# Performance work log

Hardware: AMD Instinct MI355X
Metric: run time of the kernel (lower is better)

Reference implementation:

```python
import jax, jax.numpy as jnp
import numpy as np
import math

B, CIN, H, W = 32, 128, 64, 64
COUT, KH, KW = 256, 3, 3


def setup_inputs() -> dict:
    key = jax.random.key(0)
    k1, k2, k3 = jax.random.split(key, 3)
    sqrtk = math.sqrt(1.0 / (CIN * KH * KW))
    x = jax.random.normal(k1, (B, CIN, H, W), dtype=jnp.float32)
    weight = jax.random.uniform(k2, (COUT, CIN, KH, KW), dtype=jnp.float32, minval=-sqrtk, maxval=sqrtk)
    bias = jax.random.uniform(k3, (COUT,), dtype=jnp.float32, minval=-sqrtk, maxval=sqrtk)
    return {"input": x, "weight": weight, "bias": bias}


def reference(input, weight, bias):
    # VALID (no padding), stride-1 cross-correlation conv, NCHW/OIHW layout,
    # matching the original nested-loop direct convolution + per-channel bias.
    out = jax.lax.conv_general_dilated(
        input, weight,
        window_strides=(1, 1), padding='VALID',
        dimension_numbers=('NCHW', 'OIHW', 'NCHW'))
    return out + bias[None, :, None, None]
```

## Files before the change

kernel.cpp:

```cpp
#include <hip/hip_runtime.h>

#define NB   32
#define NCI  128
#define NH   64
#define NW   64
#define NCO  256
#define NOH  62
#define NOW  62

typedef __attribute__((ext_vector_type(8))) short bf16x8;
typedef __attribute__((ext_vector_type(8))) unsigned short u16x8;
typedef __attribute__((ext_vector_type(4))) float f32x4;

typedef __attribute__((address_space(1))) const unsigned int glb_u32_t;
typedef __attribute__((address_space(3))) unsigned int lds_u32_t;

__device__ __forceinline__ unsigned short f2bf(float f) {
  unsigned int u = __float_as_uint(f);
  u = u + 0x7FFFu + ((u >> 16) & 1u);
  return (unsigned short)(u >> 16);
}

__device__ __forceinline__ void gload_lds16(const unsigned short* g, unsigned short* l) {
  __builtin_amdgcn_global_load_lds((glb_u32_t*)g, (lds_u32_t*)l, 16, 0, 0);
}

__global__ __launch_bounds__(256) void cvt_w_kernel(const float* __restrict__ wsrc,
                                                    unsigned short* __restrict__ wt) {
  int t = blockIdx.x * 256 + threadIdx.x;
  int oc = t & 15, co = (t >> 4) & 255, k = t >> 12;
  const float* src = wsrc + ((size_t)co * NCI + oc * 8) * 9 + k;
  u16x8 v;
  #pragma unroll
  for (int j = 0; j < 8; ++j) v[j] = f2bf(src[j * 9]);
  *(u16x8*)(wt + ((size_t)k * NCO + co) * NCI + oc * 8) = v;
}

__global__ __launch_bounds__(256, 2) void conv_mfma_kernel(
    const float* __restrict__ x, const unsigned short* __restrict__ wt,
    const float* __restrict__ bias, float* __restrict__ out) {
  __shared__ unsigned short smem[40960];

  const int tid  = threadIdx.x;
  const int lane = tid & 63;
  const int wid  = tid >> 6;
  const int wn   = wid;
  const int l15  = lane & 15;
  const int lo   = lane >> 4;

  const int bid0  = blockIdx.x;
  const int bid   = (bid0 & 7) * 128 + (bid0 >> 3);
  const int coutg = bid & 1;
  const int ohg   = (bid >> 1) & 15;
  const int b     = bid >> 5;
  const int cbase = coutg * 128;
  const int oh0   = ohg * 4;

  f32x4 acc[8][4];
  #pragma unroll
  for (int mi = 0; mi < 8; ++mi)
    #pragma unroll
    for (int ni = 0; ni < 4; ++ni)
      acc[mi][ni] = (f32x4){0.f, 0.f, 0.f, 0.f};

  const char* sm = (const char*)smem;
  const int af_lane = l15 * 64 + ((lo ^ ((l15 >> 1) & 3)) << 4);

  const float* xb = x + ((size_t)b * NCI) * (NH * NW);

  const unsigned short* wsrc2[2];
  #pragma unroll
  for (int i = 0; i < 2; ++i) {
    int e = (wid * 2 + i) * 64 + lane;
    int o = e & 3, co = e >> 2;
    wsrc2[i] = wt + (size_t)(cbase + co) * NCI + ((o ^ ((co >> 1) & 3)) * 8);
  }

  auto stage_w = [&](int t) {
    unsigned short* dst = smem + 24576 + (t & 3) * 4096;
    const size_t so = (size_t)(t % 9) * NCO * NCI + (t / 9) * 32;
    #pragma unroll
    for (int i = 0; i < 2; ++i)
      gload_lds16(wsrc2[i] + so, dst + ((wid * 2 + i) * 64 + lane) * 8);
  };

  auto xload8 = [&](int c1, int uu, float (&xf)[8]) {
    const int g = uu * 4 + wid;
    const int r = g % 6, oct = g / 6;
    int row = oh0 + r; if (row > 63) row = 63;
    const float* src = xb + (size_t)(c1 * 32 + oct * 8) * (NH * NW)
                     + row * NW + lane;
    #pragma unroll
    for (int j = 0; j < 8; ++j) xf[j] = src[(size_t)j * (NH * NW)];
  };
  auto xwrite8 = [&](int c1, int uu, float (&xf)[8]) {
    const int g = uu * 4 + wid;
    const int r = g % 6, oct = g / 6;
    u16x8 v;
    #pragma unroll
    for (int j = 0; j < 8; ++j) v[j] = f2bf(xf[j]);
    *(u16x8*)(smem + (c1 & 1) * 12288 +
              ((r * 64 + lane) * 4 + (oct ^ ((lane >> 1) & 3))) * 8) = v;
  };

  bf16x8 afX[4], afY[4], bfC[4];

  {
    float xa[8], xbv[8], xc[8], xd[8], xe[8], xg[8];
    xload8(0, 0, xa); xload8(0, 1, xbv); xload8(0, 2, xc);
    xload8(0, 3, xd); xload8(0, 4, xe);  xload8(0, 5, xg);
    stage_w(0); stage_w(1); stage_w(2);
    asm volatile("s_waitcnt vmcnt(6)" ::: "memory");
    xwrite8(0, 0, xa); xwrite8(0, 1, xbv); xwrite8(0, 2, xc);
    xwrite8(0, 3, xd); xwrite8(0, 4, xe);  xwrite8(0, 5, xg);
    asm volatile("s_waitcnt vmcnt(0) lgkmcnt(0)" ::: "memory");
    __builtin_amdgcn_s_barrier();
    __builtin_amdgcn_sched_barrier(0);
    const char* wsp0 = sm + 49152;
    #pragma unroll
    for (int i = 0; i < 4; ++i)
      afX[i] = *(const bf16x8*)(wsp0 + i * 1024 + af_lane);
    const char* xsp0 = sm + wn * 4096;
    #pragma unroll
    for (int i = 0; i < 4; ++i)
      bfC[i] = *(const bf16x8*)(xsp0 + i * 1024 + af_lane);
  }

  for (int t = 0; t < 36; ++t) {
    const int t9 = t % 9, c = t / 9;
    const bool xst = (t9 >= 2 && t9 <= 7) && (c < 3);
    const bool pf  = (t < 35);
    float xf[8];

    if (xst) xload8(c + 1, t9 - 2, xf);
    __builtin_amdgcn_sched_barrier(0);
    if (t + 3 < 36) stage_w(t + 3);
    __builtin_amdgcn_sched_barrier(0);

    const char* wsp  = sm + 49152 + (t & 3) * 8192;
    const char* wspn = sm + 49152 + ((t + 1) & 3) * 8192;

    asm volatile("s_waitcnt lgkmcnt(0)" ::: "memory");
    __builtin_amdgcn_sched_barrier(0);
    __builtin_amdgcn_s_setprio(1);
    #pragma unroll
    for (int ni = 0; ni < 4; ++ni)
      acc[0][ni] = __builtin_amdgcn_mfma_f32_16x16x32_bf16(afX[0], bfC[ni], acc[0][ni], 0, 0, 0);
    afY[0] = *(const bf16x8*)(wsp + 4 * 1024 + af_lane);
    afY[1] = *(const bf16x8*)(wsp + 5 * 1024 + af_lane);
    #pragma unroll
    for (int ni = 0; ni < 4; ++ni)
      acc[1][ni] = __builtin_amdgcn_mfma_f32_16x16x32_bf16(afX[1], bfC[ni], acc[1][ni], 0, 0, 0);
    afY[2] = *(const bf16x8*)(wsp + 6 * 1024 + af_lane);
    afY[3] = *(const bf16x8*)(wsp + 7 * 1024 + af_lane);
    #pragma unroll
    for (int ni = 0; ni < 4; ++ni)
      acc[2][ni] = __builtin_amdgcn_mfma_f32_16x16x32_bf16(afX[2], bfC[ni], acc[2][ni], 0, 0, 0);
    #pragma unroll
    for (int ni = 0; ni < 4; ++ni)
      acc[3][ni] = __builtin_amdgcn_mfma_f32_16x16x32_bf16(afX[3], bfC[ni], acc[3][ni], 0, 0, 0);
    __builtin_amdgcn_s_setprio(0);

    asm volatile("s_waitcnt lgkmcnt(0)" ::: "memory");
    __builtin_amdgcn_sched_barrier(0);
    __builtin_amdgcn_s_setprio(1);
    #pragma unroll
    for (int ni = 0; ni < 4; ++ni)
      acc[4][ni] = __builtin_amdgcn_mfma_f32_16x16x32_bf16(afY[0], bfC[ni], acc[4][ni], 0, 0, 0);
    if (pf) {
      afX[0] = *(const bf16x8*)(wspn + 0 * 1024 + af_lane);
      afX[1] = *(const bf16x8*)(wspn + 1 * 1024 + af_lane);
    }
    #pragma unroll
    for (int ni = 0; ni < 4; ++ni)
      acc[5][ni] = __builtin_amdgcn_mfma_f32_16x16x32_bf16(afY[1], bfC[ni], acc[5][ni], 0, 0, 0);
    if (pf) {
      afX[2] = *(const bf16x8*)(wspn + 2 * 1024 + af_lane);
      afX[3] = *(const bf16x8*)(wspn + 3 * 1024 + af_lane);
    }
    #pragma unroll
    for (int ni = 0; ni < 4; ++ni)
      acc[6][ni] = __builtin_amdgcn_mfma_f32_16x16x32_bf16(afY[2], bfC[ni], acc[6][ni], 0, 0, 0);
    #pragma unroll
    for (int ni = 0; ni < 4; ++ni)
      acc[7][ni] = __builtin_amdgcn_mfma_f32_16x16x32_bf16(afY[3], bfC[ni], acc[7][ni], 0, 0, 0);
    __builtin_amdgcn_s_setprio(0);

    if (t >= 33) {
      asm volatile("s_waitcnt vmcnt(0)" ::: "memory");
    } else {
      asm volatile("s_waitcnt vmcnt(2)" ::: "memory");
    }
    if (xst) xwrite8(c + 1, t9 - 2, xf);
    if (pf) {
      const int tn = t + 1, tn9 = tn % 9, cn = tn / 9;
      const int khn = tn9 / 3, kwn = tn9 - khn * 3;
      const char* xspn = sm + (cn & 1) * 24576 + (wn + khn) * 4096;
      const int w9n = l15 + kwn;
      const int bfln = w9n * 64 + ((lo ^ ((w9n >> 1) & 3)) << 4);
      #pragma unroll
      for (int i = 0; i < 4; ++i)
        bfC[i] = *(const bf16x8*)(xspn + i * 1024 + bfln);
    }
    if (xst) asm volatile("s_waitcnt lgkmcnt(4)" ::: "memory");
    __builtin_amdgcn_s_barrier();
    __builtin_amdgcn_sched_barrier(0);
  }

  const int oh = oh0 + wn;
  if (oh < NOH) {
    #pragma unroll
    for (int mi = 0; mi < 8; ++mi) {
      int co0 = cbase + mi * 16 + lo * 4;
      const f32x4 bv = *(const f32x4*)(bias + co0);
      #pragma unroll
      for (int ni = 0; ni < 4; ++ni) {
        int ow = ni * 16 + l15;
        if (ow < NOW) {
          size_t o0 = (((size_t)b * NCO + co0) * NOH + oh) * NOW + ow;
          const size_t cs = (size_t)NOH * NOW;
          out[o0]          = acc[mi][ni][0] + bv[0];
          out[o0 + cs]     = acc[mi][ni][1] + bv[1];
          out[o0 + 2 * cs] = acc[mi][ni][2] + bv[2];
          out[o0 + 3 * cs] = acc[mi][ni][3] + bv[3];
        }
      }
    }
  }
}

__global__ __launch_bounds__(256) void conv_naive_kernel(
    const float* __restrict__ x, const float* __restrict__ w,
    const float* __restrict__ bias, float* __restrict__ out) {
  long t = (long)blockIdx.x * 256 + threadIdx.x;
  const long total = (long)NB * NCO * NOH * NOW;
  if (t >= total) return;
  int ow = (int)(t % NOW);
  int oh = (int)((t / NOW) % NOH);
  int co = (int)((t / ((long)NOW * NOH)) % NCO);
  int b  = (int)(t / ((long)NOW * NOH * NCO));
  float acc = bias[co];
  for (int ci = 0; ci < NCI; ++ci) {
    const float* xp = x + (((size_t)b * NCI + ci) * NH + oh) * NW + ow;
    const float* wp = w + ((size_t)co * NCI + ci) * 9;
    #pragma unroll
    for (int kh = 0; kh < 3; ++kh)
      #pragma unroll
      for (int kw = 0; kw < 3; ++kw)
        acc += xp[kh * NW + kw] * wp[kh * 3 + kw];
  }
  out[t] = acc;
}

extern "C" void kernel_launch(void* const* d_in, const int* in_sizes, int n_in,
                              void* d_out, int out_size, void* d_ws, size_t ws_size,
                              hipStream_t stream) {
  const float* x    = (const float*)d_in[0];
  const float* w    = (const float*)d_in[1];
  const float* bias = (const float*)d_in[2];
  float* out        = (float*)d_out;

  const size_t WT_BYTES = (size_t)9 * NCO * NCI * 2;

  if (ws_size >= WT_BYTES) {
    unsigned short* wt = (unsigned short*)d_ws;
    cvt_w_kernel<<<(9 * NCO * 16) / 256, 256, 0, stream>>>(w, wt);
    conv_mfma_kernel<<<2 * 16 * NB, 256, 0, stream>>>(x, wt, bias, out);
  } else {
    const long total = (long)NB * NCO * NOH * NOW;
    conv_naive_kernel<<<(int)((total + 255) / 256), 256, 0, stream>>>(x, w, bias, out);
  }
}
```

Baseline: 88.83 us.

## Switch conv main loop to 32x32x16 bf16 MFMA with double-buffered B fragments

Replaces the 16x16x32 MFMA tiling (8x4 accumulators) with 32x32x16 MFMA (4x2 accumulators of 16 floats). The LDS fragment addressing and the output epilogue are remapped to match. The tap loop becomes a lambda unrolled four times and ping-pongs two B-fragment register sets, so next-tap input fragments load during the current MFMAs rather than after them. The aim is fewer MFMA issues and fewer LDS reads per tap, with B-fragment load latency hidden. In exchange the larger unrolled body may raise register pressure, and the new swizzle mapping must stay correct.

```diff
diff --git a/kernel.cpp b/kernel.cpp
--- a/kernel.cpp
+++ b/kernel.cpp
@@ -8,9 +8,10 @@
 #define NOH  62
 #define NOW  62
 
-typedef __attribute__((ext_vector_type(8))) short bf16x8;
-typedef __attribute__((ext_vector_type(8))) unsigned short u16x8;
-typedef __attribute__((ext_vector_type(4))) float f32x4;
+typedef __attribute__((ext_vector_type(8)))  short bf16x8;
+typedef __attribute__((ext_vector_type(8)))  unsigned short u16x8;
+typedef __attribute__((ext_vector_type(4)))  float f32x4;
+typedef __attribute__((ext_vector_type(16))) float f32x16;
 
 typedef __attribute__((address_space(1))) const unsigned int glb_u32_t;
 typedef __attribute__((address_space(3))) unsigned int lds_u32_t;
@@ -45,8 +46,8 @@
   const int lane = tid & 63;
   const int wid  = tid >> 6;
   const int wn   = wid;
-  const int l15  = lane & 15;
-  const int lo   = lane >> 4;
+  const int l31  = lane & 31;
+  const int lo5  = lane >> 5;
 
   const int bid0  = blockIdx.x;
   const int bid   = (bid0 & 7) * 128 + (bid0 >> 3);
@@ -56,15 +57,16 @@
   const int cbase = coutg * 128;
   const int oh0   = ohg * 4;
 
-  f32x4 acc[8][4];
+  f32x16 acc[4][2];
   #pragma unroll
-  for (int mi = 0; mi < 8; ++mi)
-    #pragma unroll
-    for (int ni = 0; ni < 4; ++ni)
-      acc[mi][ni] = (f32x4){0.f, 0.f, 0.f, 0.f};
+  for (int mi = 0; mi < 4; ++mi)
+    #pragma unroll
+    for (int ni = 0; ni < 2; ++ni)
+      acc[mi][ni] = (f32x16)(0.f);
 
   const char* sm = (const char*)smem;
-  const int af_lane = l15 * 64 + ((lo ^ ((l15 >> 1) & 3)) << 4);
+  const int afb0 = l31 * 64 + ((lo5 ^ ((l31 >> 1) & 3)) << 4);
+  const int afb1 = afb0 ^ 32;
 
   const float* xb = x + ((size_t)b * NCI) * (NH * NW);
 
@@ -103,7 +105,73 @@
               ((r * 64 + lane) * 4 + (oct ^ ((lane >> 1) & 3))) * 8) = v;
   };
 
-  bf16x8 afX[4], afY[4], bfC[4];
+  bf16x8 afX[4], afY[4], bfC[4], bfD[4];
+
+  auto tap_body = [&](int t, bf16x8 (&bfc)[4], bf16x8 (&bfn)[4], bool pf) {
+    const int t9 = t % 9, c = t / 9;
+    const bool xst = (t9 >= 2 && t9 <= 7) && (c < 3);
+    float xf[8];
+
+    if (xst) xload8(c + 1, t9 - 2, xf);
+    __builtin_amdgcn_sched_barrier(0);
+    if (t + 3 < 36) stage_w(t + 3);
+    __builtin_amdgcn_sched_barrier(0);
+
+    const char* wsp  = sm + 49152 + (t & 3) * 8192;
+    const char* wspn = sm + 49152 + ((t + 1) & 3) * 8192;
+    const int tn = t + 1, tn9 = tn % 9, cn = tn / 9;
+    const int khn = tn9 / 3, kwn = tn9 - khn * 3;
+    const char* xspn = sm + (cn & 1) * 24576 + (wn + khn) * 4096;
+    const int w9n  = l31 + kwn;
+    const int bfln = w9n * 64 + ((lo5 ^ ((w9n >> 1) & 3)) << 4);
+
+    asm volatile("s_waitcnt lgkmcnt(0)" ::: "memory");
+    __builtin_amdgcn_sched_barrier(0);
+    __builtin_amdgcn_s_setprio(1);
+    acc[0][0] = __builtin_amdgcn_mfma_f32_32x32x16_bf16(afX[0], bfc[0], acc[0][0], 0, 0, 0);
+    afY[0] = *(const bf16x8*)(wsp + 0 * 2048 + afb1);
+    afY[1] = *(const bf16x8*)(wsp + 1 * 2048 + afb1);
+    acc[0][1] = __builtin_amdgcn_mfma_f32_32x32x16_bf16(afX[0], bfc[1], acc[0][1], 0, 0, 0);
+    afY[2] = *(const bf16x8*)(wsp + 2 * 2048 + afb1);
+    afY[3] = *(const bf16x8*)(wsp + 3 * 2048 + afb1);
+    acc[1][0] = __builtin_amdgcn_mfma_f32_32x32x16_bf16(afX[1], bfc[0], acc[1][0], 0, 0, 0);
+    acc[1][1] = __builtin_amdgcn_mfma_f32_32x32x16_bf16(afX[1], bfc[1], acc[1][1], 0, 0, 0);
+    acc[2][0] = __builtin_amdgcn_mfma_f32_32x32x16_bf16(afX[2], bfc[0], acc[2][0], 0, 0, 0);
+    acc[2][1] = __builtin_amdgcn_mfma_f32_32x32x16_bf16(afX[2], bfc[1], acc[2][1], 0, 0, 0);
+    acc[3][0] = __builtin_amdgcn_mfma_f32_32x32x16_bf16(afX[3], bfc[0], acc[3][0], 0, 0, 0);
+    acc[3][1] = __builtin_amdgcn_mfma_f32_32x32x16_bf16(afX[3], bfc[1], acc[3][1], 0, 0, 0);
+    __builtin_amdgcn_s_setprio(0);
+
+    asm volatile("s_waitcnt lgkmcnt(0)" ::: "memory");
+    __builtin_amdgcn_sched_barrier(0);
+    __builtin_amdgcn_s_setprio(1);
+    acc[0][0] = __builtin_amdgcn_mfma_f32_32x32x16_bf16(afY[0], bfc[2], acc[0][0], 0, 0, 0);
+    if (pf) { afX[0] = *(const bf16x8*)(wspn + 0 * 2048 + afb0);
+              afX[1] = *(const bf16x8*)(wspn + 1 * 2048 + afb0); }
+    acc[0][1] = __builtin_amdgcn_mfma_f32_32x32x16_bf16(afY[0], bfc[3], acc[0][1], 0, 0, 0);
+    if (pf) { afX[2] = *(const bf16x8*)(wspn + 2 * 2048 + afb0);
+              afX[3] = *(const bf16x8*)(wspn + 3 * 2048 + afb0); }
+    acc[1][0] = __builtin_amdgcn_mfma_f32_32x32x16_bf16(afY[1], bfc[2], acc[1][0], 0, 0, 0);
+    if (pf) { bfn[0] = *(const bf16x8*)(xspn + bfln);
+              bfn[1] = *(const bf16x8*)(xspn + 2048 + bfln); }
+    acc[1][1] = __builtin_amdgcn_mfma_f32_32x32x16_bf16(afY[1], bfc[3], acc[1][1], 0, 0, 0);
+    if (pf) { bfn[2] = *(const bf16x8*)(xspn + (bfln ^ 32));
+              bfn[3] = *(const bf16x8*)(xspn + 2048 + (bfln ^ 32)); }
+    acc[2][0] = __builtin_amdgcn_mfma_f32_32x32x16_bf16(afY[2], bfc[2], acc[2][0], 0, 0, 0);
+    acc[2][1] = __builtin_amdgcn_mfma_f32_32x32x16_bf16(afY[2], bfc[3], acc[2][1], 0, 0, 0);
+    acc[3][0] = __builtin_amdgcn_mfma_f32_32x32x16_bf16(afY[3], bfc[2], acc[3][0], 0, 0, 0);
+    acc[3][1] = __builtin_amdgcn_mfma_f32_32x32x16_bf16(afY[3], bfc[3], acc[3][1], 0, 0, 0);
+    __builtin_amdgcn_s_setprio(0);
+
+    if (t >= 33) { asm volatile("s_waitcnt vmcnt(0)" ::: "memory"); }
+    else         { asm volatile("s_waitcnt vmcnt(2)" ::: "memory"); }
+    if (xst) {
+      xwrite8(c + 1, t9 - 2, xf);
+      asm volatile("s_waitcnt lgkmcnt(0)" ::: "memory");
+    }
+    __builtin_amdgcn_s_barrier();
+    __builtin_amdgcn_sched_barrier(0);
+  };
 
   {
     float xa[8], xbv[8], xc[8], xd[8], xe[8], xg[8];
@@ -118,114 +186,46 @@
     __builtin_amdgcn_sched_barrier(0);
     const char* wsp0 = sm + 49152;
     #pragma unroll
-    for (int i = 0; i < 4; ++i)
-      afX[i] = *(const bf16x8*)(wsp0 + i * 1024 + af_lane);
+    for (int mi = 0; mi < 4; ++mi)
+      afX[mi] = *(const bf16x8*)(wsp0 + mi * 2048 + afb0);
     const char* xsp0 = sm + wn * 4096;
-    #pragma unroll
-    for (int i = 0; i < 4; ++i)
-      bfC[i] = *(const bf16x8*)(xsp0 + i * 1024 + af_lane);
-  }
-
-  for (int t = 0; t < 36; ++t) {
-    const int t9 = t % 9, c = t / 9;
-    const bool xst = (t9 >= 2 && t9 <= 7) && (c < 3);
-    const bool pf  = (t < 35);
-    float xf[8];
-
-    if (xst) xload8(c + 1, t9 - 2, xf);
-    __builtin_amdgcn_sched_barrier(0);
-    if (t + 3 < 36) stage_w(t + 3);
-    __builtin_amdgcn_sched_barrier(0);
-
-    const char* wsp  = sm + 49152 + (t & 3) * 8192;
-    const char* wspn = sm + 49152 + ((t + 1) & 3) * 8192;
-
-    asm volatile("s_waitcnt lgkmcnt(0)" ::: "memory");
-    __builtin_amdgcn_sched_barrier(0);
-    __builtin_amdgcn_s_setprio(1);
-    #pragma unroll
-    for (int ni = 0; ni < 4; ++ni)
-      acc[0][ni] = __builtin_amdgcn_mfma_f32_16x16x32_bf16(afX[0], bfC[ni], acc[0][ni], 0, 0, 0);
-    afY[0] = *(const bf16x8*)(wsp + 4 * 1024 + af_lane);
-    afY[1] = *(const bf16x8*)(wsp + 5 * 1024 + af_lane);
-    #pragma unroll
-    for (int ni = 0; ni < 4; ++ni)
-      acc[1][ni] = __builtin_amdgcn_mfma_f32_16x16x32_bf16(afX[1], bfC[ni], acc[1][ni], 0, 0, 0);
-    afY[2] = *(const bf16x8*)(wsp + 6 * 1024 + af_lane);
-    afY[3] = *(const bf16x8*)(wsp + 7 * 1024 + af_lane);
-    #pragma unroll
-    for (int ni = 0; ni < 4; ++ni)
-      acc[2][ni] = __builtin_amdgcn_mfma_f32_16x16x32_bf16(afX[2], bfC[ni], acc[2][ni], 0, 0, 0);
-    #pragma unroll
-    for (int ni = 0; ni < 4; ++ni)
-      acc[3][ni] = __builtin_amdgcn_mfma_f32_16x16x32_bf16(afX[3], bfC[ni], acc[3][ni], 0, 0, 0);
-    __builtin_amdgcn_s_setprio(0);
-
-    asm volatile("s_waitcnt lgkmcnt(0)" ::: "memory");
-    __builtin_amdgcn_sched_barrier(0);
-    __builtin_amdgcn_s_setprio(1);
-    #pragma unroll
-    for (int ni = 0; ni < 4; ++ni)
-      acc[4][ni] = __builtin_amdgcn_mfma_f32_16x16x32_bf16(afY[0], bfC[ni], acc[4][ni], 0, 0, 0);
-    if (pf) {
-      afX[0] = *(const bf16x8*)(wspn + 0 * 1024 + af_lane);
-      afX[1] = *(const bf16x8*)(wspn + 1 * 1024 + af_lane);
-    }
-    #pragma unroll
-    for (int ni = 0; ni < 4; ++ni)
-      acc[5][ni] = __builtin_amdgcn_mfma_f32_16x16x32_bf16(afY[1], bfC[ni], acc[5][ni], 0, 0, 0);
-    if (pf) {
-      afX[2] = *(const bf16x8*)(wspn + 2 * 1024 + af_lane);
-      afX[3] = *(const bf16x8*)(wspn + 3 * 1024 + af_lane);
-    }
-    #pragma unroll
-    for (int ni = 0; ni < 4; ++ni)
-      acc[6][ni] = __builtin_amdgcn_mfma_f32_16x16x32_bf16(afY[2], bfC[ni], acc[6][ni], 0, 0, 0);
-    #pragma unroll
-    for (int ni = 0; ni < 4; ++ni)
-      acc[7][ni] = __builtin_amdgcn_mfma_f32_16x16x32_bf16(afY[3], bfC[ni], acc[7][ni], 0, 0, 0);
-    __builtin_amdgcn_s_setprio(0);
-
-    if (t >= 33) {
-      asm volatile("s_waitcnt vmcnt(0)" ::: "memory");
-    } else {
-      asm volatile("s_waitcnt vmcnt(2)" ::: "memory");
-    }
-    if (xst) xwrite8(c + 1, t9 - 2, xf);
-    if (pf) {
-      const int tn = t + 1, tn9 = tn % 9, cn = tn / 9;
-      const int khn = tn9 / 3, kwn = tn9 - khn * 3;
-      const char* xspn = sm + (cn & 1) * 24576 + (wn + khn) * 4096;
-      const int w9n = l15 + kwn;
-      const int bfln = w9n * 64 + ((lo ^ ((w9n >> 1) & 3)) << 4);
-      #pragma unroll
-      for (int i = 0; i < 4; ++i)
-        bfC[i] = *(const bf16x8*)(xspn + i * 1024 + bfln);
-    }
-    if (xst) asm volatile("s_waitcnt lgkmcnt(4)" ::: "memory");
-    __builtin_amdgcn_s_barrier();
-    __builtin_amdgcn_sched_barrier(0);
+    const int bfl0 = l31 * 64 + ((lo5 ^ ((l31 >> 1) & 3)) << 4);
+    bfC[0] = *(const bf16x8*)(xsp0 + bfl0);
+    bfC[1] = *(const bf16x8*)(xsp0 + 2048 + bfl0);
+    bfC[2] = *(const bf16x8*)(xsp0 + (bfl0 ^ 32));
+    bfC[3] = *(const bf16x8*)(xsp0 + 2048 + (bfl0 ^ 32));
+  }
+
+  for (int j = 0; j < 9; ++j) {
+    const int t0 = 4 * j;
+    tap_body(t0 + 0, bfC, bfD, true);
+    tap_body(t0 + 1, bfD, bfC, true);
+    tap_body(t0 + 2, bfC, bfD, true);
+    tap_body(t0 + 3, bfD, bfC, j < 8);
   }
 
   const int oh = oh0 + wn;
   if (oh < NOH) {
-    #pragma unroll
-    for (int mi = 0; mi < 8; ++mi) {
-      int co0 = cbase + mi * 16 + lo * 4;
-      const f32x4 bv = *(const f32x4*)(bias + co0);
+    const int ow0 = l31;
+    #pragma unroll
+    for (int mi = 0; mi < 4; ++mi)
       #pragma unroll
-      for (int ni = 0; ni < 4; ++ni) {
-        int ow = ni * 16 + l15;
+      for (int ni = 0; ni < 2; ++ni) {
+        int ow = ni * 32 + ow0;
         if (ow < NOW) {
-          size_t o0 = (((size_t)b * NCO + co0) * NOH + oh) * NOW + ow;
-          const size_t cs = (size_t)NOH * NOW;
-          out[o0]          = acc[mi][ni][0] + bv[0];
-          out[o0 + cs]     = acc[mi][ni][1] + bv[1];
-          out[o0 + 2 * cs] = acc[mi][ni][2] + bv[2];
-          out[o0 + 3 * cs] = acc[mi][ni][3] + bv[3];
+          #pragma unroll
+          for (int rg = 0; rg < 4; ++rg) {
+            int co0 = cbase + mi * 32 + 8 * rg + 4 * lo5;
+            const f32x4 bv = *(const f32x4*)(bias + co0);
+            size_t o0 = (((size_t)b * NCO + co0) * NOH + oh) * NOW + ow;
+            const size_t cs = (size_t)NOH * NOW;
+            out[o0]          = acc[mi][ni][4 * rg + 0] + bv[0];
+            out[o0 + cs]     = acc[mi][ni][4 * rg + 1] + bv[1];
+            out[o0 + 2 * cs] = acc[mi][ni][4 * rg + 2] + bv[2];
+            out[o0 + 3 * cs] = acc[mi][ni][4 * rg + 3] + bv[3];
+          }
         }
       }
-    }
   }
 }
 
```

Result: no change. 89.18 us (+0.4%).

## Load conv weights directly into registers and drop per-tap barriers

Applied to the files above, without the earlier changes.

Repacks the bf16 weights into a per-tap, per-channel-chunk, MFMA-fragment-friendly layout. Each wave then loads its A fragments straight from global memory into double-buffered registers instead of staging them through LDS. This shrinks LDS to the input double buffer only, and block barriers now happen once per 32-channel chunk instead of every tap. The trade-off is that all four waves fetch the same weight fragments redundantly from global/L2 each tap, and the weight loads are exposed to global latency rather than LDS latency.

```diff
diff --git a/kernel.cpp b/kernel.cpp
--- a/kernel.cpp
+++ b/kernel.cpp
@@ -12,34 +12,27 @@
 typedef __attribute__((ext_vector_type(8))) unsigned short u16x8;
 typedef __attribute__((ext_vector_type(4))) float f32x4;
 
-typedef __attribute__((address_space(1))) const unsigned int glb_u32_t;
-typedef __attribute__((address_space(3))) unsigned int lds_u32_t;
-
 __device__ __forceinline__ unsigned short f2bf(float f) {
   unsigned int u = __float_as_uint(f);
   u = u + 0x7FFFu + ((u >> 16) & 1u);
   return (unsigned short)(u >> 16);
 }
 
-__device__ __forceinline__ void gload_lds16(const unsigned short* g, unsigned short* l) {
-  __builtin_amdgcn_global_load_lds((glb_u32_t*)g, (lds_u32_t*)l, 16, 0, 0);
-}
-
 __global__ __launch_bounds__(256) void cvt_w_kernel(const float* __restrict__ wsrc,
-                                                    unsigned short* __restrict__ wt) {
+                                                    unsigned short* __restrict__ wt2) {
   int t = blockIdx.x * 256 + threadIdx.x;
-  int oc = t & 15, co = (t >> 4) & 255, k = t >> 12;
-  const float* src = wsrc + ((size_t)co * NCI + oc * 8) * 9 + k;
+  int oct = t & 3, cic = (t >> 2) & 3, co = (t >> 4) & 255, tap = t >> 12;
+  const float* src = wsrc + ((size_t)(co * 128 + cic * 32 + oct * 8)) * 9 + tap;
   u16x8 v;
   #pragma unroll
   for (int j = 0; j < 8; ++j) v[j] = f2bf(src[j * 9]);
-  *(u16x8*)(wt + ((size_t)k * NCO + co) * NCI + oc * 8) = v;
+  *(u16x8*)(wt2 + (((size_t)(tap * 4 + cic) * 256 + co) * 4 + oct) * 8) = v;
 }
 
 __global__ __launch_bounds__(256, 2) void conv_mfma_kernel(
-    const float* __restrict__ x, const unsigned short* __restrict__ wt,
+    const float* __restrict__ x, const unsigned short* __restrict__ wt2,
     const float* __restrict__ bias, float* __restrict__ out) {
-  __shared__ unsigned short smem[40960];
+  __shared__ unsigned short smem[24576];
 
   const int tid  = threadIdx.x;
   const int lane = tid & 63;
@@ -64,24 +57,27 @@
       acc[mi][ni] = (f32x4){0.f, 0.f, 0.f, 0.f};
 
   const char* sm = (const char*)smem;
-  const int af_lane = l15 * 64 + ((lo ^ ((l15 >> 1) & 3)) << 4);
+  const char* wb = (const char*)wt2;
+  const int alo = (cbase + l15) * 64 + lo * 16;
 
   const float* xb = x + ((size_t)b * NCI) * (NH * NW);
 
-  const unsigned short* wsrc2[2];
-  #pragma unroll
-  for (int i = 0; i < 2; ++i) {
-    int e = (wid * 2 + i) * 64 + lane;
-    int o = e & 3, co = e >> 2;
-    wsrc2[i] = wt + (size_t)(cbase + co) * NCI + ((o ^ ((co >> 1) & 3)) * 8);
-  }
-
-  auto stage_w = [&](int t) {
-    unsigned short* dst = smem + 24576 + (t & 3) * 4096;
-    const size_t so = (size_t)(t % 9) * NCO * NCI + (t / 9) * 32;
-    #pragma unroll
-    for (int i = 0; i < 2; ++i)
-      gload_lds16(wsrc2[i] + so, dst + ((wid * 2 + i) * 64 + lane) * 8);
+  auto load_af = [&](bf16x8 (&dst)[8], int t) {
+    const char* p = wb + (size_t)((t % 9) * 4 + t / 9) * 16384 + alo;
+    #pragma unroll
+    for (int mi = 0; mi < 8; ++mi)
+      dst[mi] = *(const bf16x8*)(p + mi * 1024);
+  };
+
+  auto read_bf = [&](bf16x8 (&dst)[4], int t) {
+    const int t9 = t % 9, cn = t / 9;
+    const int kh = t9 / 3, kw = t9 - kh * 3;
+    const char* xsp = sm + (cn & 1) * 24576 + (wn + kh) * 4096;
+    const int w9 = l15 + kw;
+    const int bfl = w9 * 64 + ((lo ^ ((w9 >> 1) & 3)) << 4);
+    #pragma unroll
+    for (int ni = 0; ni < 4; ++ni)
+      dst[ni] = *(const bf16x8*)(xsp + ni * 1024 + bfl);
   };
 
   auto xload8 = [&](int c1, int uu, float (&xf)[8]) {
@@ -103,108 +99,65 @@
               ((r * 64 + lane) * 4 + (oct ^ ((lane >> 1) & 3))) * 8) = v;
   };
 
-  bf16x8 afX[4], afY[4], bfC[4];
+  bf16x8 afA[8], afB[8], bfC[4];
+  float xf[8];
+
+  auto tap_body = [&](bf16x8 (&afU)[8], bf16x8 (&afN)[8], int t) {
+    const int t9 = t % 9, c = t / 9;
+    const bool xsPrev = (t >= 1) && ((t - 1) % 9 <= 5) && ((t - 1) / 9 < 3);
+    const bool xsCur  = (t9 <= 5) && (c < 3);
+
+    if (xsPrev) { asm volatile("s_waitcnt vmcnt(8)" ::: "memory"); }
+    else        { asm volatile("s_waitcnt vmcnt(0)" ::: "memory"); }
+    asm volatile("s_waitcnt lgkmcnt(0)" ::: "memory");
+    __builtin_amdgcn_sched_barrier(0);
+
+    if (t < 35) load_af(afN, t + 1);
+    __builtin_amdgcn_sched_barrier(0);
+
+    __builtin_amdgcn_s_setprio(1);
+    #pragma unroll
+    for (int mi = 0; mi < 8; ++mi)
+      #pragma unroll
+      for (int ni = 0; ni < 4; ++ni)
+        acc[mi][ni] = __builtin_amdgcn_mfma_f32_16x16x32_bf16(
+            afU[mi], bfC[ni], acc[mi][ni], 0, 0, 0);
+    __builtin_amdgcn_s_setprio(0);
+
+    if (t < 35 && (t + 1) % 9 != 0) read_bf(bfC, t + 1);
+
+    if (xsPrev) {
+      if (t < 35) { asm volatile("s_waitcnt vmcnt(8)" ::: "memory"); }
+      else        { asm volatile("s_waitcnt vmcnt(0)" ::: "memory"); }
+      xwrite8((t - 1) / 9 + 1, (t - 1) % 9, xf);
+    }
+    if (xsCur) xload8(c + 1, t9, xf);
+
+    if (t9 == 8 && c < 3) {
+      asm volatile("s_waitcnt lgkmcnt(0)" ::: "memory");
+      __builtin_amdgcn_s_barrier();
+      __builtin_amdgcn_sched_barrier(0);
+      read_bf(bfC, t + 1);
+    }
+  };
 
   {
-    float xa[8], xbv[8], xc[8], xd[8], xe[8], xg[8];
-    xload8(0, 0, xa); xload8(0, 1, xbv); xload8(0, 2, xc);
-    xload8(0, 3, xd); xload8(0, 4, xe);  xload8(0, 5, xg);
-    stage_w(0); stage_w(1); stage_w(2);
-    asm volatile("s_waitcnt vmcnt(6)" ::: "memory");
-    xwrite8(0, 0, xa); xwrite8(0, 1, xbv); xwrite8(0, 2, xc);
-    xwrite8(0, 3, xd); xwrite8(0, 4, xe);  xwrite8(0, 5, xg);
+    float x6[6][8];
+    #pragma unroll
+    for (int u = 0; u < 6; ++u) xload8(0, u, x6[u]);
+    load_af(afA, 0);
+    asm volatile("s_waitcnt vmcnt(8)" ::: "memory");
+    #pragma unroll
+    for (int u = 0; u < 6; ++u) xwrite8(0, u, x6[u]);
     asm volatile("s_waitcnt vmcnt(0) lgkmcnt(0)" ::: "memory");
     __builtin_amdgcn_s_barrier();
     __builtin_amdgcn_sched_barrier(0);
-    const char* wsp0 = sm + 49152;
-    #pragma unroll
-    for (int i = 0; i < 4; ++i)
-      afX[i] = *(const bf16x8*)(wsp0 + i * 1024 + af_lane);
-    const char* xsp0 = sm + wn * 4096;
-    #pragma unroll
-    for (int i = 0; i < 4; ++i)
-      bfC[i] = *(const bf16x8*)(xsp0 + i * 1024 + af_lane);
-  }
-
-  for (int t = 0; t < 36; ++t) {
-    const int t9 = t % 9, c = t / 9;
-    const bool xst = (t9 >= 2 && t9 <= 7) && (c < 3);
-    const bool pf  = (t < 35);
-    float xf[8];
-
-    if (xst) xload8(c + 1, t9 - 2, xf);
-    __builtin_amdgcn_sched_barrier(0);
-    if (t + 3 < 36) stage_w(t + 3);
-    __builtin_amdgcn_sched_barrier(0);
-
-    const char* wsp  = sm + 49152 + (t & 3) * 8192;
-    const char* wspn = sm + 49152 + ((t + 1) & 3) * 8192;
-
-    asm volatile("s_waitcnt lgkmcnt(0)" ::: "memory");
-    __builtin_amdgcn_sched_barrier(0);
-    __builtin_amdgcn_s_setprio(1);
-    #pragma unroll
-    for (int ni = 0; ni < 4; ++ni)
-      acc[0][ni] = __builtin_amdgcn_mfma_f32_16x16x32_bf16(afX[0], bfC[ni], acc[0][ni], 0, 0, 0);
-    afY[0] = *(const bf16x8*)(wsp + 4 * 1024 + af_lane);
-    afY[1] = *(const bf16x8*)(wsp + 5 * 1024 + af_lane);
-    #pragma unroll
-    for (int ni = 0; ni < 4; ++ni)
-      acc[1][ni] = __builtin_amdgcn_mfma_f32_16x16x32_bf16(afX[1], bfC[ni], acc[1][ni], 0, 0, 0);
-    afY[2] = *(const bf16x8*)(wsp + 6 * 1024 + af_lane);
-    afY[3] = *(const bf16x8*)(wsp + 7 * 1024 + af_lane);
-    #pragma unroll
-    for (int ni = 0; ni < 4; ++ni)
-      acc[2][ni] = __builtin_amdgcn_mfma_f32_16x16x32_bf16(afX[2], bfC[ni], acc[2][ni], 0, 0, 0);
-    #pragma unroll
-    for (int ni = 0; ni < 4; ++ni)
-      acc[3][ni] = __builtin_amdgcn_mfma_f32_16x16x32_bf16(afX[3], bfC[ni], acc[3][ni], 0, 0, 0);
-    __builtin_amdgcn_s_setprio(0);
-
-    asm volatile("s_waitcnt lgkmcnt(0)" ::: "memory");
-    __builtin_amdgcn_sched_barrier(0);
-    __builtin_amdgcn_s_setprio(1);
-    #pragma unroll
-    for (int ni = 0; ni < 4; ++ni)
-      acc[4][ni] = __builtin_amdgcn_mfma_f32_16x16x32_bf16(afY[0], bfC[ni], acc[4][ni], 0, 0, 0);
-    if (pf) {
-      afX[0] = *(const bf16x8*)(wspn + 0 * 1024 + af_lane);
-      afX[1] = *(const bf16x8*)(wspn + 1 * 1024 + af_lane);
-    }
-    #pragma unroll
-    for (int ni = 0; ni < 4; ++ni)
-      acc[5][ni] = __builtin_amdgcn_mfma_f32_16x16x32_bf16(afY[1], bfC[ni], acc[5][ni], 0, 0, 0);
-    if (pf) {
-      afX[2] = *(const bf16x8*)(wspn + 2 * 1024 + af_lane);
-      afX[3] = *(const bf16x8*)(wspn + 3 * 1024 + af_lane);
-    }
-    #pragma unroll
-    for (int ni = 0; ni < 4; ++ni)
-      acc[6][ni] = __builtin_amdgcn_mfma_f32_16x16x32_bf16(afY[2], bfC[ni], acc[6][ni], 0, 0, 0);
-    #pragma unroll
-    for (int ni = 0; ni < 4; ++ni)
-      acc[7][ni] = __builtin_amdgcn_mfma_f32_16x16x32_bf16(afY[3], bfC[ni], acc[7][ni], 0, 0, 0);
-    __builtin_amdgcn_s_setprio(0);
-
-    if (t >= 33) {
-      asm volatile("s_waitcnt vmcnt(0)" ::: "memory");
-    } else {
-      asm volatile("s_waitcnt vmcnt(2)" ::: "memory");
-    }
-    if (xst) xwrite8(c + 1, t9 - 2, xf);
-    if (pf) {
-      const int tn = t + 1, tn9 = tn % 9, cn = tn / 9;
-      const int khn = tn9 / 3, kwn = tn9 - khn * 3;
-      const char* xspn = sm + (cn & 1) * 24576 + (wn + khn) * 4096;
-      const int w9n = l15 + kwn;
-      const int bfln = w9n * 64 + ((lo ^ ((w9n >> 1) & 3)) << 4);
-      #pragma unroll
-      for (int i = 0; i < 4; ++i)
-        bfC[i] = *(const bf16x8*)(xspn + i * 1024 + bfln);
-    }
-    if (xst) asm volatile("s_waitcnt lgkmcnt(4)" ::: "memory");
-    __builtin_amdgcn_s_barrier();
-    __builtin_amdgcn_sched_barrier(0);
+    read_bf(bfC, 0);
+  }
+
+  for (int h = 0; h < 18; ++h) {
+    tap_body(afA, afB, 2 * h);
+    tap_body(afB, afA, 2 * h + 1);
   }
 
   const int oh = oh0 + wn;
@@ -260,12 +213,12 @@
   const float* bias = (const float*)d_in[2];
   float* out        = (float*)d_out;
 
-  const size_t WT_BYTES = (size_t)9 * NCO * NCI * 2;
+  const size_t WT_BYTES = (size_t)9 * 4 * NCO * 4 * 8 * 2;
 
   if (ws_size >= WT_BYTES) {
-    unsigned short* wt = (unsigned short*)d_ws;
-    cvt_w_kernel<<<(9 * NCO * 16) / 256, 256, 0, stream>>>(w, wt);
-    conv_mfma_kernel<<<2 * 16 * NB, 256, 0, stream>>>(x, wt, bias, out);
+    unsigned short* wt2 = (unsigned short*)d_ws;
+    cvt_w_kernel<<<144, 256, 0, stream>>>(w, wt2);
+    conv_mfma_kernel<<<2 * 16 * NB, 256, 0, stream>>>(x, wt2, bias, out);
   } else {
     const long total = (long)NB * NCO * NOH * NOW;
     conv_naive_kernel<<<(int)((total + 255) / 256), 256, 0, stream>>>(x, w, bias, out);
```

After: 108.7 us. 1.22x slower.
